# Kernel tuning notes

Measured on AMD Instinct MI355X. Metric: run time of the kernel, lower is better.

## Reference

```python
import jax, jax.numpy as jnp
import numpy as np

D_IN = 1024
D_OUT = 1024


def setup_inputs() -> dict:
    key = jax.random.key(0)
    kx, kq, kk, kv = jax.random.split(key, 4)
    x = jax.random.normal(kx, (4, 2048, D_IN), dtype=jnp.float32)
    # nn.Linear weight has shape [d_out, d_in]; y = x @ W.T
    s = 1.0 / np.sqrt(D_IN)
    W_query = jax.random.uniform(kq, (D_OUT, D_IN), jnp.float32, -s, s)
    W_key = jax.random.uniform(kk, (D_OUT, D_IN), jnp.float32, -s, s)
    W_value = jax.random.uniform(kv, (D_OUT, D_IN), jnp.float32, -s, s)
    return {"x": x, "W_query": W_query, "W_key": W_key, "W_value": W_value}


def reference(x, W_query, W_key, W_value):
    # x: [b, n, d_in]; W_*: [d_out, d_in]
    q = jnp.einsum("bnd,kd->bnk", x, W_query)
    k = jnp.einsum("bnd,kd->bnk", x, W_key)
    v = jnp.einsum("bnd,kd->bnk", x, W_value)
    d_k = W_query.shape[0]
    scores = jnp.einsum("bqk,bnk->bqn", q, k) * (d_k ** -0.5)  # [b, n, n]
    weights = jax.nn.softmax(scores, axis=-1)
    return jnp.einsum("bqn,bnk->bqk", weights, v)
```

## Files before the change

### kernel.cpp

```cpp
#include <hip/hip_runtime.h>
#include <hip/hip_bf16.h>
#include <stdint.h>


typedef __attribute__((ext_vector_type(8))) short bf16x8;
typedef __attribute__((ext_vector_type(4))) float f32x4;

__device__ __forceinline__ void async_copy16(const void* g, void* l) {
  __builtin_amdgcn_global_load_lds(
      (__attribute__((address_space(1))) void*)(g),
      (__attribute__((address_space(3))) void*)(l),
      16, 0, 0);
}

template<int NI, int NT, int KS>
__device__ __forceinline__ void mainloop256(
    const __hip_bfloat16* __restrict__ aS,
    const __hip_bfloat16* __restrict__ bS,
    __hip_bfloat16* As, __hip_bfloat16* Bs,
    const int wid, const int wm, const int wn,
    const int l16, const int quad, const int sw,
    f32x4 (&acc)[8][NI])
{
  const bf16x8* Av = (const bf16x8*)As;
  const bf16x8* Bv = (const bf16x8*)Bs;
  char* lA = (char*)As + wid * 1024;
  char* lB = (char*)Bs + wid * 1024;
  bf16x8 bfr[NI][2];
  bf16x8 afc[2][2], afn[2][2];

#define SB0 __builtin_amdgcn_sched_barrier(0)

#define STG_A2(t) do { \
    _Pragma("unroll") \
    for (int p = 0; p < 4; ++p) \
      async_copy16(aS + ((t)*64 + (long long)p * 64 * KS), \
                   lA + ((t)&1)*32768 + p * 64 * 128); \
  } while (0)
#define STG_B2(t) do { \
    _Pragma("unroll") \
    for (int p = 0; p < NI; ++p) \
      async_copy16(bS + ((t)*64 + (long long)p * 64 * KS), \
                   lB + ((t)&1)*(NI*8192) + p * 64 * 128); \
  } while (0)

#define RD_AF(dst, t, phi) do { \
    _Pragma("unroll") \
    for (int m2 = 0; m2 < 2; ++m2) \
      _Pragma("unroll") \
      for (int kk = 0; kk < 2; ++kk) \
        dst[m2][kk] = Av[((t)&1)*2048 + (wm + ((phi)*2 + m2)*16 + l16)*8 + ((kk*4 + quad) ^ sw)]; \
  } while (0)
#define RD_BF(t, nlo, nhi) do { \
    _Pragma("unroll") \
    for (int ni = (nlo); ni < (nhi); ++ni) \
      _Pragma("unroll") \
      for (int kk = 0; kk < 2; ++kk) \
        bfr[ni][kk] = Bv[((t)&1)*(NI*512) + (wn + ni*16 + l16)*8 + ((kk*4 + quad) ^ sw)]; \
  } while (0)
#define MM(src, phi, nlo, nhi) do { \
    _Pragma("unroll") \
    for (int kk = 0; kk < 2; ++kk) \
      _Pragma("unroll") \
      for (int m2 = 0; m2 < 2; ++m2) \
        _Pragma("unroll") \
        for (int ni = (nlo); ni < (nhi); ++ni) \
          acc[(phi)*2 + m2][ni] = __builtin_amdgcn_mfma_f32_16x16x32_bf16( \
              src[m2][kk], bfr[ni][kk], acc[(phi)*2 + m2][ni], 0, 0, 0); \
  } while (0)

#define GATE0 do { SB0; \
    asm volatile("s_waitcnt vmcnt(0)" ::: "memory"); } while (0)
#define GNONE (void)0

#define TILE(t, STG_STMT, GATE_STMT) do { \
    RD_BF(t, 0, NI); \
    RD_AF(afc, t, 0); \
    RD_AF(afn, t, 1); \
    STG_STMT; \
    __builtin_amdgcn_s_setprio(1); MM(afc, 0, 0, NI); __builtin_amdgcn_s_setprio(0); \
    RD_AF(afc, t, 2); \
    __builtin_amdgcn_s_setprio(1); \
    MM(afn, 1, 0, NI); \
    __builtin_amdgcn_s_setprio(0); \
    RD_AF(afn, t, 3); \
    __builtin_amdgcn_s_setprio(1); \
    MM(afc, 2, 0, NI); \
    MM(afn, 3, 0, NI); \
    __builtin_amdgcn_s_setprio(0); \
    GATE_STMT; \
    SB0; \
    __builtin_amdgcn_s_barrier(); \
  } while (0)

  STG_B2(0); STG_A2(0);
  GATE0;
  __builtin_amdgcn_s_barrier();

  #pragma unroll 1
  for (int i = 0; i < NT / 2 - 1; ++i) {
    const int ta = 2 * i, tb = 2 * i + 1;
    TILE(ta, { STG_A2(ta + 1); STG_B2(ta + 1); }, GATE0);
    TILE(tb, { STG_A2(tb + 1); STG_B2(tb + 1); }, GATE0);
  }
  TILE(NT - 2, { STG_A2(NT - 1); STG_B2(NT - 1); }, GATE0);
  TILE(NT - 1, GNONE, GNONE);

#undef TILE
#undef GATE0
#undef GNONE
#undef MM
#undef RD_BF
#undef RD_AF
#undef STG_A2
#undef STG_B2
#undef SB0
}

__global__ __launch_bounds__(512, 2)
void gemm_qk(const __hip_bfloat16* __restrict__ A,
             const __hip_bfloat16* __restrict__ B,
             __hip_bfloat16* __restrict__ Q,
             __hip_bfloat16* __restrict__ Kk)
{
  __shared__ __align__(16) __hip_bfloat16 As[2][256 * 64];
  __shared__ __align__(16) __hip_bfloat16 Bs[2][256 * 64];

  const int bid = blockIdx.x;
  const int s   = (bid & 7) * 32 + (bid >> 3);
  const long long tile_m = (long long)(s >> 3) * 256;
  const long long tile_n = (long long)(s & 7) * 256;

  const int tid  = threadIdx.x;
  const int wid  = tid >> 6;
  const int lane = tid & 63;
  const int srow = wid * 8 + (lane >> 3);
  const int scol = ((lane & 7) ^ (lane >> 3)) * 8;

  const __hip_bfloat16* aS = A + (tile_m + srow) * 1024 + scol;
  const __hip_bfloat16* bS = B + (tile_n + srow) * 1024 + scol;

  const int wm   = (wid >> 2) * 128;
  const int wn   = (wid & 3) * 64;
  const int quad = lane >> 4;
  const int l16  = lane & 15;
  const int sw   = l16 & 7;

  f32x4 acc[8][4];
  #pragma unroll
  for (int mi = 0; mi < 8; ++mi)
    #pragma unroll
    for (int ni = 0; ni < 4; ++ni)
      acc[mi][ni] = (f32x4){0.f, 0.f, 0.f, 0.f};

  mainloop256<4, 16, 1024>(aS, bS, &As[0][0], &Bs[0][0],
                           wid, wm, wn, l16, quad, sw, acc);

  const int mat = (int)(tile_n >> 10);
  __hip_bfloat16* outp = (mat == 0) ? Q : Kk;
  const float scale = (mat == 0) ? 0.03125f : 1.0f;
  const int coln0 = (int)(tile_n & 1023);
  #pragma unroll
  for (int mi = 0; mi < 8; ++mi) {
    #pragma unroll
    for (int r = 0; r < 4; ++r) {
      const long long row = tile_m + wm + mi * 16 + quad * 4 + r;
      #pragma unroll
      for (int ni = 0; ni < 4; ++ni) {
        const int col = coln0 + wn + ni * 16 + l16;
        outp[row * 1024 + col] = __float2bfloat16(acc[mi][ni][r] * scale);
      }
    }
  }
}

__global__ __launch_bounds__(512, 2)
void gemm_v(const __hip_bfloat16* __restrict__ A,
            const __hip_bfloat16* __restrict__ B,
            __hip_bfloat16* __restrict__ Vt)
{
  __shared__ __align__(16) __hip_bfloat16 As[2][256 * 64];
  __shared__ __align__(16) __hip_bfloat16 Bs[2][128 * 64];

  const int bid = blockIdx.x;
  const int s   = (bid & 7) * 32 + (bid >> 3);
  const long long tile_m = (long long)(s >> 3) * 256;
  const long long tile_n = (long long)(s & 7) * 128;

  const int tid  = threadIdx.x;
  const int wid  = tid >> 6;
  const int lane = tid & 63;
  const int srow = wid * 8 + (lane >> 3);
  const int scol = ((lane & 7) ^ (lane >> 3)) * 8;

  const __hip_bfloat16* aS = A + (tile_m + srow) * 1024 + scol;
  const __hip_bfloat16* bS = B + (tile_n + srow) * 1024 + scol;

  const int wm   = (wid >> 2) * 128;
  const int wn   = (wid & 3) * 32;
  const int quad = lane >> 4;
  const int l16  = lane & 15;
  const int sw   = l16 & 7;

  f32x4 acc[8][2];
  #pragma unroll
  for (int mi = 0; mi < 8; ++mi)
    #pragma unroll
    for (int ni = 0; ni < 2; ++ni)
      acc[mi][ni] = (f32x4){0.f, 0.f, 0.f, 0.f};

  mainloop256<2, 16, 1024>(aS, bS, &As[0][0], &Bs[0][0],
                           wid, wm, wn, l16, quad, sw, acc);

  const int b    = (int)(tile_m >> 11);
  const int seq0 = (int)(tile_m & 2047);
  const int d0   = (int)tile_n;
  #pragma unroll
  for (int mi = 0; mi < 8; ++mi) {
    const int seq = seq0 + wm + mi * 16 + quad * 4;
    #pragma unroll
    for (int ni = 0; ni < 2; ++ni) {
      const int d = d0 + wn + ni * 16 + l16;
      union { ushort4 u; unsigned short sh[4]; } pk;
      #pragma unroll
      for (int r = 0; r < 4; ++r)
        pk.sh[r] = __bfloat16_as_ushort(__float2bfloat16(acc[mi][ni][r]));
      *(ushort4*)(Vt + ((long long)(b * 1024 + d)) * 2048 + seq) = pk.u;
    }
  }
}

__global__ __launch_bounds__(512, 2)
void gemm_s_exp(const __hip_bfloat16* __restrict__ A,
                const __hip_bfloat16* __restrict__ B,
                __hip_bfloat16* __restrict__ Cout,
                float* __restrict__ part)
{
  __shared__ __align__(16) __hip_bfloat16 As[2][256 * 64];
  __shared__ __align__(16) __hip_bfloat16 Bs[2][256 * 64];

  const int u   = blockIdx.x + (blockIdx.y << 3) + (blockIdx.z << 6);
  const int xcd = u & 7;
  const int rr  = u >> 3;
  const int bz  = xcd >> 1;
  const int tmi = ((xcd & 1) << 2) + (rr >> 3);
  const int tni = rr & 7;

  A += (long long)bz * 2048 * 1024;
  B += (long long)bz * 2048 * 1024;

  const long long tile_m = (long long)tmi * 256;
  const long long tile_n = (long long)tni * 256;

  const int tid  = threadIdx.x;
  const int wid  = tid >> 6;
  const int lane = tid & 63;
  const int srow = wid * 8 + (lane >> 3);
  const int scol = ((lane & 7) ^ (lane >> 3)) * 8;

  const __hip_bfloat16* aS = A + (tile_m + srow) * 1024 + scol;
  const __hip_bfloat16* bS = B + (tile_n + srow) * 1024 + scol;

  const int wm   = (wid >> 2) * 128;
  const int wn   = (wid & 3) * 64;
  const int quad = lane >> 4;
  const int l16  = lane & 15;
  const int sw   = l16 & 7;

  f32x4 acc[8][4];
  #pragma unroll
  for (int mi = 0; mi < 8; ++mi)
    #pragma unroll
    for (int ni = 0; ni < 4; ++ni)
      acc[mi][ni] = (f32x4){0.f, 0.f, 0.f, 0.f};

  mainloop256<4, 16, 1024>(aS, bS, &As[0][0], &Bs[0][0],
                           wid, wm, wn, l16, quad, sw, acc);

  __hip_bfloat16* C = Cout + (long long)bz * 2048 * 2048;
  #pragma unroll
  for (int mi = 0; mi < 8; ++mi) {
    #pragma unroll
    for (int r = 0; r < 4; ++r) {
      const long long row = tile_m + wm + mi * 16 + quad * 4 + r;
      float ssum = 0.f;
      #pragma unroll
      for (int ni = 0; ni < 4; ++ni) {
        const float e = __expf(acc[mi][ni][r]);
        const __hip_bfloat16 h = __float2bfloat16(e);
        C[row * 2048 + tile_n + wn + ni * 16 + l16] = h;
        ssum += __bfloat162float(h);
      }
      #pragma unroll
      for (int off = 1; off < 16; off <<= 1) ssum += __shfl_xor(ssum, off, 64);
      if (l16 == 0)
        part[((long long)bz * 2048 + row) * 32 + tni * 4 + (wid & 3)] = ssum;
    }
  }
}

__global__ __launch_bounds__(512, 2)
void gemm_pv(const __hip_bfloat16* __restrict__ A,
             const __hip_bfloat16* __restrict__ B,
             const float* __restrict__ part,
             float* __restrict__ Cout)
{
  __shared__ __align__(16) __hip_bfloat16 As[2][256 * 64];
  __shared__ __align__(16) __hip_bfloat16 Bs[2][128 * 64];
  __shared__ float rinv[256];

  const int u   = blockIdx.x + (blockIdx.y << 3) + (blockIdx.z << 6);
  const int xcd = u & 7;
  const int rr  = u >> 3;
  const int bz  = xcd >> 1;
  const int tmi = ((xcd & 1) << 2) + (rr >> 3);
  const int tni = rr & 7;

  A += (long long)bz * 2048 * 2048;
  B += (long long)bz * 1024 * 2048;

  const long long tile_m = (long long)tmi * 256;
  const long long tile_n = (long long)tni * 128;

  const int tid  = threadIdx.x;
  const int wid  = tid >> 6;
  const int lane = tid & 63;
  const int srow = wid * 8 + (lane >> 3);
  const int scol = ((lane & 7) ^ (lane >> 3)) * 8;

  const __hip_bfloat16* aS = A + (tile_m + srow) * 2048 + scol;
  const __hip_bfloat16* bS = B + (tile_n + srow) * 2048 + scol;

  const int wm   = (wid >> 2) * 128;
  const int wn   = (wid & 3) * 32;
  const int quad = lane >> 4;
  const int l16  = lane & 15;
  const int sw   = l16 & 7;

  f32x4 acc[8][2];
  #pragma unroll
  for (int mi = 0; mi < 8; ++mi)
    #pragma unroll
    for (int ni = 0; ni < 2; ++ni)
      acc[mi][ni] = (f32x4){0.f, 0.f, 0.f, 0.f};

  mainloop256<2, 32, 2048>(aS, bS, &As[0][0], &Bs[0][0],
                           wid, wm, wn, l16, quad, sw, acc);

  if (tid < 256) {
    const float4* pp = (const float4*)(part + ((long long)bz * 2048 + tile_m + tid) * 32);
    float s = 0.f;
    #pragma unroll
    for (int j = 0; j < 8; ++j) {
      const float4 f = pp[j];
      s += f.x + f.y + f.z + f.w;
    }
    rinv[tid] = 1.f / s;
  }
  __syncthreads();

  float* C = Cout + (long long)bz * 2048 * 1024;
  #pragma unroll
  for (int mi = 0; mi < 8; ++mi) {
    #pragma unroll
    for (int r = 0; r < 4; ++r) {
      const int rloc = wm + mi * 16 + quad * 4 + r;
      const float inv = rinv[rloc];
      const long long row = tile_m + rloc;
      #pragma unroll
      for (int ni = 0; ni < 2; ++ni) {
        const long long col = tile_n + wn + ni * 16 + l16;
        C[row * 1024 + col] = acc[mi][ni][r] * inv;
      }
    }
  }
}

__global__ __launch_bounds__(256)
void cast_all(const float* __restrict__ x,
              const float* __restrict__ Wq, const float* __restrict__ Wk,
              const float* __restrict__ Wv,
              __hip_bfloat16* __restrict__ xb, __hip_bfloat16* __restrict__ wcat)
{
  const int bx = blockIdx.x;
  const float* src;
  __hip_bfloat16* dst;
  int i;
  if (bx < 8192) {
    src = x; dst = xb; i = bx * 256 + threadIdx.x;
  } else {
    const int which = (bx - 8192) >> 10;
    src = (which == 0) ? Wq : (which == 1) ? Wk : Wv;
    dst = wcat + (long long)which * 1048576;
    i = ((bx - 8192) & 1023) * 256 + threadIdx.x;
  }
  const float4 f = ((const float4*)src)[i];
  union { ushort4 u; __hip_bfloat16 h[4]; } r;
  r.h[0] = __float2bfloat16(f.x);
  r.h[1] = __float2bfloat16(f.y);
  r.h[2] = __float2bfloat16(f.z);
  r.h[3] = __float2bfloat16(f.w);
  ((ushort4*)dst)[i] = r.u;
}

extern "C" void kernel_launch(void* const* d_in, const int* in_sizes, int n_in,
                              void* d_out, int out_size, void* d_ws, size_t ws_size,
                              hipStream_t stream)
{
  (void)in_sizes; (void)n_in; (void)out_size; (void)ws_size;

  const float* x  = (const float*)d_in[0];
  const float* Wq = (const float*)d_in[1];
  const float* Wk = (const float*)d_in[2];
  const float* Wv = (const float*)d_in[3];
  float* out = (float*)d_out;

  char* ws = (char*)d_ws;
  __hip_bfloat16* xb   = (__hip_bfloat16*)(ws);
  float*          part = (float*)(ws);
  __hip_bfloat16* wcat = (__hip_bfloat16*)(ws + (16LL << 20));
  __hip_bfloat16* Q    = (__hip_bfloat16*)(ws + (22LL << 20));
  __hip_bfloat16* Kk   = (__hip_bfloat16*)(ws + (38LL << 20));
  __hip_bfloat16* Vt   = (__hip_bfloat16*)(ws + (54LL << 20));
  __hip_bfloat16* S    = (__hip_bfloat16*)(ws + (70LL << 20));

  cast_all<<<11264, 256, 0, stream>>>(x, Wq, Wk, Wv, xb, wcat);

  gemm_qk<<<256, 512, 0, stream>>>(xb, wcat, Q, Kk);

  gemm_v<<<256, 512, 0, stream>>>(xb, wcat + 2097152, Vt);

  gemm_s_exp<<<dim3(8, 8, 4), 512, 0, stream>>>(Q, Kk, S, part);

  gemm_pv<<<dim3(8, 8, 4), 512, 0, stream>>>(S, Vt, part, out);
}
```

Before: 220.9 us.

## Triple-buffer LDS in V and PV GEMMs with two-tile-ahead prefetch

Adds a triple-buffered main loop for the 256x128 GEMM tiles (V projection and PV product). Global-to-LDS copies now run two K-tiles ahead and wait with vmcnt(6) instead of draining all loads every tile. The goal is to hide global load latency behind MFMA work. In exchange, LDS use per block rises to about 144KB, which may cut blocks per CU below the launch bound of 2 and lower occupancy.

```diff
diff --git a/kernel.cpp b/kernel.cpp
--- a/kernel.cpp
+++ b/kernel.cpp
@@ -12,6 +12,8 @@
       (__attribute__((address_space(3))) void*)(l),
       16, 0, 0);
 }
+
+#define SB0 __builtin_amdgcn_sched_barrier(0)
 
 template<int NI, int NT, int KS>
 __device__ __forceinline__ void mainloop256(
@@ -29,8 +31,6 @@
   bf16x8 bfr[NI][2];
   bf16x8 afc[2][2], afn[2][2];
 
-#define SB0 __builtin_amdgcn_sched_barrier(0)
-
 #define STG_A2(t) do { \
     _Pragma("unroll") \
     for (int p = 0; p < 4; ++p) \
@@ -43,7 +43,6 @@
       async_copy16(bS + ((t)*64 + (long long)p * 64 * KS), \
                    lB + ((t)&1)*(NI*8192) + p * 64 * 128); \
   } while (0)
-
 #define RD_AF(dst, t, phi) do { \
     _Pragma("unroll") \
     for (int m2 = 0; m2 < 2; ++m2) \
@@ -68,7 +67,6 @@
           acc[(phi)*2 + m2][ni] = __builtin_amdgcn_mfma_f32_16x16x32_bf16( \
               src[m2][kk], bfr[ni][kk], acc[(phi)*2 + m2][ni], 0, 0, 0); \
   } while (0)
-
 #define GATE0 do { SB0; \
     asm volatile("s_waitcnt vmcnt(0)" ::: "memory"); } while (0)
 #define GNONE (void)0
@@ -114,7 +112,105 @@
 #undef RD_AF
 #undef STG_A2
 #undef STG_B2
-#undef SB0
+}
+
+template<int NT, int KS>
+__device__ __forceinline__ void mainloop128tb(
+    const __hip_bfloat16* __restrict__ aS,
+    const __hip_bfloat16* __restrict__ bS,
+    __hip_bfloat16* As, __hip_bfloat16* Bs,
+    const int wid, const int wm, const int wn,
+    const int l16, const int quad, const int sw,
+    f32x4 (&acc)[8][2])
+{
+  const bf16x8* Av = (const bf16x8*)As;
+  const bf16x8* Bv = (const bf16x8*)Bs;
+  char* lA = (char*)As + wid * 1024;
+  char* lB = (char*)Bs + wid * 1024;
+  bf16x8 bfr[2][2];
+  bf16x8 afc[2][2], afn[2][2];
+
+#define STG_A3(t, bw) do { \
+    _Pragma("unroll") \
+    for (int p = 0; p < 4; ++p) \
+      async_copy16(aS + ((t)*64 + (long long)p * 64 * KS), \
+                   lA + (bw)*32768 + p * 64 * 128); \
+  } while (0)
+#define STG_B3(t, bw) do { \
+    _Pragma("unroll") \
+    for (int p = 0; p < 2; ++p) \
+      async_copy16(bS + ((t)*64 + (long long)p * 64 * KS), \
+                   lB + (bw)*16384 + p * 64 * 128); \
+  } while (0)
+#define RD_AF3(dst, br, phi) do { \
+    _Pragma("unroll") \
+    for (int m2 = 0; m2 < 2; ++m2) \
+      _Pragma("unroll") \
+      for (int kk = 0; kk < 2; ++kk) \
+        dst[m2][kk] = Av[(br)*2048 + (wm + ((phi)*2 + m2)*16 + l16)*8 + ((kk*4 + quad) ^ sw)]; \
+  } while (0)
+#define RD_BF3(br) do { \
+    _Pragma("unroll") \
+    for (int ni = 0; ni < 2; ++ni) \
+      _Pragma("unroll") \
+      for (int kk = 0; kk < 2; ++kk) \
+        bfr[ni][kk] = Bv[(br)*1024 + (wn + ni*16 + l16)*8 + ((kk*4 + quad) ^ sw)]; \
+  } while (0)
+#define MM3(src, phi) do { \
+    _Pragma("unroll") \
+    for (int kk = 0; kk < 2; ++kk) \
+      _Pragma("unroll") \
+      for (int m2 = 0; m2 < 2; ++m2) \
+        _Pragma("unroll") \
+        for (int ni = 0; ni < 2; ++ni) \
+          acc[(phi)*2 + m2][ni] = __builtin_amdgcn_mfma_f32_16x16x32_bf16( \
+              src[m2][kk], bfr[ni][kk], acc[(phi)*2 + m2][ni], 0, 0, 0); \
+  } while (0)
+#define GATE6 do { SB0; \
+    asm volatile("s_waitcnt vmcnt(6)" ::: "memory"); } while (0)
+#define GATE0T do { SB0; \
+    asm volatile("s_waitcnt vmcnt(0)" ::: "memory"); } while (0)
+#define GNONE3 (void)0
+
+#define TILE3(t, br, STG_STMT, GATE_STMT) do { \
+    RD_BF3(br); \
+    RD_AF3(afc, br, 0); \
+    RD_AF3(afn, br, 1); \
+    STG_STMT; \
+    __builtin_amdgcn_s_setprio(1); MM3(afc, 0); __builtin_amdgcn_s_setprio(0); \
+    RD_AF3(afc, br, 2); \
+    __builtin_amdgcn_s_setprio(1); MM3(afn, 1); __builtin_amdgcn_s_setprio(0); \
+    RD_AF3(afn, br, 3); \
+    __builtin_amdgcn_s_setprio(1); MM3(afc, 2); MM3(afn, 3); __builtin_amdgcn_s_setprio(0); \
+    GATE_STMT; \
+    SB0; \
+    __builtin_amdgcn_s_barrier(); \
+  } while (0)
+
+  STG_B3(0, 0); STG_A3(0, 0); STG_B3(1, 1); STG_A3(1, 1);
+  GATE6;
+  __builtin_amdgcn_s_barrier();
+
+  int br = 0;
+  #pragma unroll 1
+  for (int t = 0; t < NT - 2; ++t) {
+    const int bw = (br + 2 >= 3) ? (br - 1) : (br + 2);
+    TILE3(t, br, { STG_A3(t + 2, bw); STG_B3(t + 2, bw); }, GATE6);
+    br = (br + 1 == 3) ? 0 : (br + 1);
+  }
+  TILE3(NT - 2, br, GNONE3, GATE0T);
+  br = (br + 1 == 3) ? 0 : (br + 1);
+  TILE3(NT - 1, br, GNONE3, GNONE3);
+
+#undef TILE3
+#undef GATE6
+#undef GATE0T
+#undef GNONE3
+#undef MM3
+#undef RD_BF3
+#undef RD_AF3
+#undef STG_A3
+#undef STG_B3
 }
 
 __global__ __launch_bounds__(512, 2)
@@ -179,8 +275,8 @@
             const __hip_bfloat16* __restrict__ B,
             __hip_bfloat16* __restrict__ Vt)
 {
-  __shared__ __align__(16) __hip_bfloat16 As[2][256 * 64];
-  __shared__ __align__(16) __hip_bfloat16 Bs[2][128 * 64];
+  __shared__ __align__(16) __hip_bfloat16 As[3][256 * 64];
+  __shared__ __align__(16) __hip_bfloat16 Bs[3][128 * 64];
 
   const int bid = blockIdx.x;
   const int s   = (bid & 7) * 32 + (bid >> 3);
@@ -209,8 +305,8 @@
     for (int ni = 0; ni < 2; ++ni)
       acc[mi][ni] = (f32x4){0.f, 0.f, 0.f, 0.f};
 
-  mainloop256<2, 16, 1024>(aS, bS, &As[0][0], &Bs[0][0],
-                           wid, wm, wn, l16, quad, sw, acc);
+  mainloop128tb<16, 1024>(aS, bS, &As[0][0], &Bs[0][0],
+                          wid, wm, wn, l16, quad, sw, acc);
 
   const int b    = (int)(tile_m >> 11);
   const int seq0 = (int)(tile_m & 2047);
@@ -305,8 +401,8 @@
              const float* __restrict__ part,
              float* __restrict__ Cout)
 {
-  __shared__ __align__(16) __hip_bfloat16 As[2][256 * 64];
-  __shared__ __align__(16) __hip_bfloat16 Bs[2][128 * 64];
+  __shared__ __align__(16) __hip_bfloat16 As[3][256 * 64];
+  __shared__ __align__(16) __hip_bfloat16 Bs[3][128 * 64];
   __shared__ float rinv[256];
 
   const int u   = blockIdx.x + (blockIdx.y << 3) + (blockIdx.z << 6);
@@ -344,8 +440,8 @@
     for (int ni = 0; ni < 2; ++ni)
       acc[mi][ni] = (f32x4){0.f, 0.f, 0.f, 0.f};
 
-  mainloop256<2, 32, 2048>(aS, bS, &As[0][0], &Bs[0][0],
-                           wid, wm, wn, l16, quad, sw, acc);
+  mainloop128tb<32, 2048>(aS, bS, &As[0][0], &Bs[0][0],
+                          wid, wm, wn, l16, quad, sw, acc);
 
   if (tid < 256) {
     const float4* pp = (const float4*)(part + ((long long)bz * 2048 + tile_m + tid) * 32);
```

Result: slower. 226.2 us (+2.4%).
